# Kernel tuning notes

Hardware: AMD Instinct MI355X
Metric: run time of the kernel (lower is better)

Reference implementation:

```python
import jax, jax.numpy as jnp
import numpy as np

L_MAX = 3
MP_SCALING = 0.1
E = 640000
N_ATOMS = 20000
K = 32


def setup_inputs() -> dict:
    key = jax.random.key(0)
    k1, k2, k3, k4, k5 = jax.random.split(key, 5)
    sh = jax.random.normal(k1, (E, (L_MAX + 1) ** 2), dtype=jnp.float32)
    radial_basis = jax.random.normal(k2, (E, L_MAX + 1, K), dtype=jnp.float32)
    center_embedding = jax.random.normal(k3, (N_ATOMS, K), dtype=jnp.float32)
    centers = jax.random.randint(k4, (E,), 0, N_ATOMS, dtype=jnp.int32)
    neighbors = jax.random.randint(k5, (E,), 0, N_ATOMS, dtype=jnp.int32)
    return {
        "sh": sh,
        "radial_basis": radial_basis,
        "center_embedding": center_embedding,
        "centers": centers,
        "neighbors": neighbors,
        "n_atoms": N_ATOMS,
    }


def reference(sh, radial_basis, center_embedding, centers, neighbors, n_atoms):
    # Gather neighbor embeddings once: [E, K]
    emb_n = center_embedding[neighbors]
    blocks = []
    off = 0
    for l in range(L_MAX + 1):
        m = 2 * l + 1
        sh_l = sh[:, off:off + m]            # [E, m]
        off += m
        rb_l = radial_basis[:, l, :]          # [E, K]
        # edge-wise product sh * radial * gathered embedding: [E, m, K]
        src = sh_l[:, :, None] * (rb_l * emb_n)[:, None, :]
        # scatter-add over center atoms -> per-atom density [n_atoms, m, K]
        dens_l = jax.ops.segment_sum(src, centers, num_segments=n_atoms)
        blocks.append(dens_l * MP_SCALING)
    # concatenate per-l blocks along the component axis: [n_atoms, sum(2l+1)=16, K]
    return jnp.concatenate(blocks, axis=1)
```

## Files before the change

kernel.cpp:

```cpp
#include <hip/hip_runtime.h>

#define KDIM 32
#define CAP 160

__global__ void scatter_slots_kernel(const int* __restrict__ centers,
                                     const int* __restrict__ neighbors,
                                     int* __restrict__ cursor,
                                     int2* __restrict__ recs, int n) {
    int i = blockIdx.x * blockDim.x + threadIdx.x;
    if (i < n) {
        int c  = centers[i];
        int nn = neighbors[i];
        int pos = atomicAdd(&cursor[c], 1);
        if (pos < CAP) recs[(size_t)c * CAP + pos] = make_int2(i, nn);
    }
}


#define EDGE_BODY(EB, RP, SHP)                                            \
    {                                                                     \
        float t0 = RP[0 * KDIM + k] * EB;                                 \
        float t1 = RP[1 * KDIM + k] * EB;                                 \
        float t2 = RP[2 * KDIM + k] * EB;                                 \
        float t3 = RP[3 * KDIM + k] * EB;                                 \
        float4 sA = SHP[0];                                               \
        float4 sB = SHP[1];                                               \
        float c0 = hb ? t2 : t0;                                          \
        float c1 = hb ? t3 : t1;                                          \
        float c2 = hb ? t3 : t2;                                          \
        a0 += sA.x * c0;                                                  \
        a1 += sA.y * c1;                                                  \
        a2 += sA.z * c1;                                                  \
        a3 += sA.w * c1;                                                  \
        a4 += sB.x * c2;                                                  \
        a5 += sB.y * c2;                                                  \
        a6 += sB.z * c2;                                                  \
        a7 += sB.w * c2;                                                  \
    }

#define GROUP4(E0, N0, E1, N1, E2, N2, E3, N3)                            \
    {                                                                     \
        float eb0 = emb[(size_t)(N0) * KDIM + k];                         \
        float eb1 = emb[(size_t)(N1) * KDIM + k];                         \
        float eb2 = emb[(size_t)(N2) * KDIM + k];                         \
        float eb3 = emb[(size_t)(N3) * KDIM + k];                         \
        const float* rp0 = rb + (size_t)(E0) * (4 * KDIM);                \
        const float* rp1 = rb + (size_t)(E1) * (4 * KDIM);                \
        const float* rp2 = rb + (size_t)(E2) * (4 * KDIM);                \
        const float* rp3 = rb + (size_t)(E3) * (4 * KDIM);                \
        const float4* sp0 = (const float4*)(sh + (size_t)(E0) * 16 + 8 * h); \
        const float4* sp1 = (const float4*)(sh + (size_t)(E1) * 16 + 8 * h); \
        const float4* sp2 = (const float4*)(sh + (size_t)(E2) * 16 + 8 * h); \
        const float4* sp3 = (const float4*)(sh + (size_t)(E3) * 16 + 8 * h); \
        EDGE_BODY(eb0, rp0, sp0)                                          \
        EDGE_BODY(eb1, rp1, sp1)                                          \
        EDGE_BODY(eb2, rp2, sp2)                                          \
        EDGE_BODY(eb3, rp3, sp3)                                          \
    }

#define RL(x, j) __builtin_amdgcn_readlane((x), (j))

__global__ __launch_bounds__(256) void imp_main_kernel(
    const float* __restrict__ sh, const float* __restrict__ rb,
    const float* __restrict__ emb, const int2* __restrict__ recs,
    const int* __restrict__ cursor, float* __restrict__ out, int n_atoms) {
    int wave = (blockIdx.x * blockDim.x + threadIdx.x) >> 6;
    int lane = threadIdx.x & 63;
    if (wave >= n_atoms) return;
    int k = lane & 31;
    int h = lane >> 5;
    bool hb = (h != 0);

    int cnt = cursor[wave];
    if (cnt > CAP) cnt = CAP;
    const int2* rbase = recs + (size_t)wave * CAP;

    float a0 = 0.f, a1 = 0.f, a2 = 0.f, a3 = 0.f;
    float a4 = 0.f, a5 = 0.f, a6 = 0.f, a7 = 0.f;

    int l8 = lane & 7;
    int i = 0;
    int2 cur = make_int2(0, 0);
    if (cnt >= 8) cur = rbase[l8];
    while (i + 8 <= cnt) {
        int2 nxt = cur;
        if (i + 16 <= cnt) nxt = rbase[i + 8 + l8];

        int e0 = RL(cur.x, 0), n0 = RL(cur.y, 0);
        int e1 = RL(cur.x, 1), n1 = RL(cur.y, 1);
        int e2 = RL(cur.x, 2), n2 = RL(cur.y, 2);
        int e3 = RL(cur.x, 3), n3 = RL(cur.y, 3);
        int e4 = RL(cur.x, 4), n4 = RL(cur.y, 4);
        int e5 = RL(cur.x, 5), n5 = RL(cur.y, 5);
        int e6 = RL(cur.x, 6), n6 = RL(cur.y, 6);
        int e7 = RL(cur.x, 7), n7 = RL(cur.y, 7);

        GROUP4(e0, n0, e1, n1, e2, n2, e3, n3)
        GROUP4(e4, n4, e5, n5, e6, n6, e7, n7)

        cur = nxt;
        i += 8;
    }
    for (; i < cnt; i++) {
        int2 r0 = rbase[i];
        int e0 = __builtin_amdgcn_readfirstlane(r0.x);
        int n0 = __builtin_amdgcn_readfirstlane(r0.y);
        float eb0 = emb[(size_t)n0 * KDIM + k];
        const float* rp0 = rb + (size_t)e0 * (4 * KDIM);
        const float4* sp0 = (const float4*)(sh + (size_t)e0 * 16 + 8 * h);
        EDGE_BODY(eb0, rp0, sp0)
    }

    const float SCALE = 0.1f;
    float* op = out + (size_t)wave * (16 * KDIM) + (size_t)(8 * h) * KDIM + k;
    op[0 * KDIM] = a0 * SCALE;
    op[1 * KDIM] = a1 * SCALE;
    op[2 * KDIM] = a2 * SCALE;
    op[3 * KDIM] = a3 * SCALE;
    op[4 * KDIM] = a4 * SCALE;
    op[5 * KDIM] = a5 * SCALE;
    op[6 * KDIM] = a6 * SCALE;
    op[7 * KDIM] = a7 * SCALE;
}

extern "C" void kernel_launch(void* const* d_in, const int* in_sizes, int n_in,
                              void* d_out, int out_size, void* d_ws, size_t ws_size,
                              hipStream_t stream) {
    const float* sh        = (const float*)d_in[0];
    const float* rb        = (const float*)d_in[1];
    const float* emb       = (const float*)d_in[2];
    const int*   centers   = (const int*)d_in[3];
    const int*   neighbors = (const int*)d_in[4];

    int E = in_sizes[3];
    int N = in_sizes[2] / KDIM;

    float* out = (float*)d_out;

    int2* recs   = (int2*)d_ws;
    int*  cursor = (int*)(recs + (size_t)N * CAP);

    hipMemsetAsync(cursor, 0, (size_t)N * sizeof(int), stream);

    scatter_slots_kernel<<<(E + 255) / 256, 256, 0, stream>>>(centers, neighbors,
                                                              cursor, recs, E);

    int blocks = (N * 64 + 255) / 256;
    imp_main_kernel<<<blocks, 256, 0, stream>>>(sh, rb, emb, recs, cursor, out, N);
}
```

Measured before the change: 547.4 us.

## Remap wave lanes to four component groups with float2 vectorized loads

Changes the lane mapping so that each wave splits into four 16-lane groups, one per block of four components, with each lane handling two K channels through float2 loads. Each lane now loads only the two radial rows it needs instead of all four, and reads four sh values instead of eight. This cuts redundant radial loads and select work per edge and vectorizes the embedding loads and output stores. In exchange the embedding row is loaded by all four groups, and fewer independent loads are batched before use.

```diff
diff --git a/kernel.cpp b/kernel.cpp
--- a/kernel.cpp
+++ b/kernel.cpp
@@ -17,45 +17,22 @@
 }
 
 
-#define EDGE_BODY(EB, RP, SHP)                                            \
+#define EDGE_BODY2(E0, N0)                                                \
     {                                                                     \
-        float t0 = RP[0 * KDIM + k] * EB;                                 \
-        float t1 = RP[1 * KDIM + k] * EB;                                 \
-        float t2 = RP[2 * KDIM + k] * EB;                                 \
-        float t3 = RP[3 * KDIM + k] * EB;                                 \
-        float4 sA = SHP[0];                                               \
-        float4 sB = SHP[1];                                               \
-        float c0 = hb ? t2 : t0;                                          \
-        float c1 = hb ? t3 : t1;                                          \
-        float c2 = hb ? t3 : t2;                                          \
-        a0 += sA.x * c0;                                                  \
-        a1 += sA.y * c1;                                                  \
-        a2 += sA.z * c1;                                                  \
-        a3 += sA.w * c1;                                                  \
-        a4 += sB.x * c2;                                                  \
-        a5 += sB.y * c2;                                                  \
-        a6 += sB.z * c2;                                                  \
-        a7 += sB.w * c2;                                                  \
-    }
-
-#define GROUP4(E0, N0, E1, N1, E2, N2, E3, N3)                            \
-    {                                                                     \
-        float eb0 = emb[(size_t)(N0) * KDIM + k];                         \
-        float eb1 = emb[(size_t)(N1) * KDIM + k];                         \
-        float eb2 = emb[(size_t)(N2) * KDIM + k];                         \
-        float eb3 = emb[(size_t)(N3) * KDIM + k];                         \
-        const float* rp0 = rb + (size_t)(E0) * (4 * KDIM);                \
-        const float* rp1 = rb + (size_t)(E1) * (4 * KDIM);                \
-        const float* rp2 = rb + (size_t)(E2) * (4 * KDIM);                \
-        const float* rp3 = rb + (size_t)(E3) * (4 * KDIM);                \
-        const float4* sp0 = (const float4*)(sh + (size_t)(E0) * 16 + 8 * h); \
-        const float4* sp1 = (const float4*)(sh + (size_t)(E1) * 16 + 8 * h); \
-        const float4* sp2 = (const float4*)(sh + (size_t)(E2) * 16 + 8 * h); \
-        const float4* sp3 = (const float4*)(sh + (size_t)(E3) * 16 + 8 * h); \
-        EDGE_BODY(eb0, rp0, sp0)                                          \
-        EDGE_BODY(eb1, rp1, sp1)                                          \
-        EDGE_BODY(eb2, rp2, sp2)                                          \
-        EDGE_BODY(eb3, rp3, sp3)                                          \
+        const float2* rpA = (const float2*)(rb + (size_t)(E0) * 128 + tA * 32 + k0); \
+        const float2* rpB = (const float2*)(rb + (size_t)(E0) * 128 + tB * 32 + k0); \
+        const float2* ep  = (const float2*)(emb + (size_t)(N0) * KDIM + k0);          \
+        const float4* sp  = (const float4*)(sh + (size_t)(E0) * 16 + 4 * h);          \
+        float2 wA = *rpA;                                                 \
+        float2 wB = *rpB;                                                 \
+        float2 em = *ep;                                                  \
+        float4 s  = *sp;                                                  \
+        wA.x *= em.x; wA.y *= em.y;                                       \
+        wB.x *= em.x; wB.y *= em.y;                                       \
+        a0x += s.x * wA.x; a0y += s.x * wA.y;                             \
+        a1x += s.y * wB.x; a1y += s.y * wB.y;                             \
+        a2x += s.z * wB.x; a2y += s.z * wB.y;                             \
+        a3x += s.w * wB.x; a3y += s.w * wB.y;                             \
     }
 
 #define RL(x, j) __builtin_amdgcn_readlane((x), (j))
@@ -67,16 +44,19 @@
     int wave = (blockIdx.x * blockDim.x + threadIdx.x) >> 6;
     int lane = threadIdx.x & 63;
     if (wave >= n_atoms) return;
-    int k = lane & 31;
-    int h = lane >> 5;
-    bool hb = (h != 0);
+    int h  = lane >> 4;
+    int kk = lane & 15;
+    int k0 = kk * 2;
+
+    int tA = (h == 0) ? 0 : ((h == 3) ? 3 : 2);
+    int tB = (h == 0) ? 1 : ((h == 1) ? 2 : 3);
 
     int cnt = cursor[wave];
     if (cnt > CAP) cnt = CAP;
     const int2* rbase = recs + (size_t)wave * CAP;
 
-    float a0 = 0.f, a1 = 0.f, a2 = 0.f, a3 = 0.f;
-    float a4 = 0.f, a5 = 0.f, a6 = 0.f, a7 = 0.f;
+    float a0x = 0.f, a0y = 0.f, a1x = 0.f, a1y = 0.f;
+    float a2x = 0.f, a2y = 0.f, a3x = 0.f, a3y = 0.f;
 
     int l8 = lane & 7;
     int i = 0;
@@ -95,8 +75,14 @@
         int e6 = RL(cur.x, 6), n6 = RL(cur.y, 6);
         int e7 = RL(cur.x, 7), n7 = RL(cur.y, 7);
 
-        GROUP4(e0, n0, e1, n1, e2, n2, e3, n3)
-        GROUP4(e4, n4, e5, n5, e6, n6, e7, n7)
+        EDGE_BODY2(e0, n0)
+        EDGE_BODY2(e1, n1)
+        EDGE_BODY2(e2, n2)
+        EDGE_BODY2(e3, n3)
+        EDGE_BODY2(e4, n4)
+        EDGE_BODY2(e5, n5)
+        EDGE_BODY2(e6, n6)
+        EDGE_BODY2(e7, n7)
 
         cur = nxt;
         i += 8;
@@ -105,22 +91,19 @@
         int2 r0 = rbase[i];
         int e0 = __builtin_amdgcn_readfirstlane(r0.x);
         int n0 = __builtin_amdgcn_readfirstlane(r0.y);
-        float eb0 = emb[(size_t)n0 * KDIM + k];
-        const float* rp0 = rb + (size_t)e0 * (4 * KDIM);
-        const float4* sp0 = (const float4*)(sh + (size_t)e0 * 16 + 8 * h);
-        EDGE_BODY(eb0, rp0, sp0)
+        EDGE_BODY2(e0, n0)
     }
 
     const float SCALE = 0.1f;
-    float* op = out + (size_t)wave * (16 * KDIM) + (size_t)(8 * h) * KDIM + k;
-    op[0 * KDIM] = a0 * SCALE;
-    op[1 * KDIM] = a1 * SCALE;
-    op[2 * KDIM] = a2 * SCALE;
-    op[3 * KDIM] = a3 * SCALE;
-    op[4 * KDIM] = a4 * SCALE;
-    op[5 * KDIM] = a5 * SCALE;
-    op[6 * KDIM] = a6 * SCALE;
-    op[7 * KDIM] = a7 * SCALE;
+    float* op = out + (size_t)wave * (16 * KDIM) + (size_t)(4 * h) * KDIM + k0;
+    float2 r0 = make_float2(a0x * SCALE, a0y * SCALE);
+    float2 r1 = make_float2(a1x * SCALE, a1y * SCALE);
+    float2 r2 = make_float2(a2x * SCALE, a2y * SCALE);
+    float2 r3 = make_float2(a3x * SCALE, a3y * SCALE);
+    *(float2*)(op + 0 * KDIM) = r0;
+    *(float2*)(op + 1 * KDIM) = r1;
+    *(float2*)(op + 2 * KDIM) = r2;
+    *(float2*)(op + 3 * KDIM) = r3;
 }
 
 extern "C" void kernel_launch(void* const* d_in, const int* in_sizes, int n_in,
```

After: 560.4 us. 1.02x slower.
